# Performance work log

Hardware: AMD Instinct MI355X
Metric: run time of the kernel (lower is better)

## Reference

```python
import jax, jax.numpy as jnp
import numpy as np

NUM_HEADS = 16
EMBED = 1024
HEAD = EMBED // NUM_HEADS  # 64
MAX_DIST = 4
NEG_INF = -1e30


def setup_inputs() -> dict:
    key = jax.random.key(0)
    ks = jax.random.split(key, 8)
    B, S = 2, 2048
    x = jax.random.normal(ks[0], (B, S, EMBED), dtype=jnp.float32)
    return {
        "k": x,  # self-attention: k == v == q values
        "v": x,
        "q": x,
        "Wk": jax.random.normal(ks[1], (EMBED, EMBED), dtype=jnp.float32) * 0.02,
        "Wv": jax.random.normal(ks[2], (EMBED, EMBED), dtype=jnp.float32) * 0.02,
        "Wq": jax.random.normal(ks[3], (EMBED, EMBED), dtype=jnp.float32) * 0.02,
        "Wo": jax.random.normal(ks[4], (EMBED, EMBED), dtype=jnp.float32) * 0.02,
        "p_params": jax.random.normal(ks[5], (HEAD, 2 * MAX_DIST + 1), dtype=jnp.float32) * 0.02,
    }


def reference(k, v, q, Wk, Wv, Wq, Wo, p_params):
    B, Kl, _ = k.shape
    Ql = q.shape[1]
    # torch nn.Linear(bias=False): y = x @ W.T
    kh = (k @ Wk.T).reshape(B, Kl, NUM_HEADS, HEAD).transpose(0, 2, 1, 3)
    vh = (v @ Wv.T).reshape(B, Kl, NUM_HEADS, HEAD).transpose(0, 2, 1, 3)
    qh = (q @ Wq.T).reshape(B, Ql, NUM_HEADS, HEAD).transpose(0, 2, 1, 3)
    qh = qh / jnp.sqrt(jnp.float32(HEAD))
    # content scores: [B,H,Q,K]
    scores0 = jnp.einsum("bhqd,bhkd->bhqk", qh, kh)
    # relative-position bias: q . p_params[:, r] for each bucket r, then gather per (i,j)
    bias = jnp.einsum("bhqd,dr->bhqr", qh, p_params)  # [B,H,Q,2M+1]
    d = jnp.clip(jnp.arange(Ql)[:, None] - jnp.arange(Kl)[None, :], -MAX_DIST, MAX_DIST) + MAX_DIST  # [Q,K]
    rel = bias[:, :, jnp.arange(Ql)[:, None], d]  # [B,H,Q,K]
    scores = scores0 + rel
    # causal mask
    causal = jnp.arange(Ql)[:, None] >= jnp.arange(Kl)[None, :]
    scores = jnp.where(causal[None, None], scores, NEG_INF)
    attn = jax.nn.softmax(scores, axis=-1)
    out = jnp.einsum("bhqk,bhkd->bhqd", attn, vh)
    out = out.transpose(0, 2, 1, 3).reshape(B, Ql, EMBED)
    return out @ Wo.T
```

## Files before the change

kernel.cpp:

```cpp
#include <hip/hip_runtime.h>


using short8  = __attribute__((ext_vector_type(8))) short;
using floatx4 = __attribute__((ext_vector_type(4))) float;
using float4v = __attribute__((ext_vector_type(4))) float;
using ushort4v = __attribute__((ext_vector_type(4))) unsigned short;
using uint2v  = __attribute__((ext_vector_type(2))) unsigned int;

#define LOG2E 1.4426950408889634f

__device__ __forceinline__ unsigned short f2bf(float f) {
  unsigned u = __float_as_uint(f);
  return (unsigned short)((u + 0x7FFFu + ((u >> 16) & 1u)) >> 16);
}
__device__ __forceinline__ float bf2f(unsigned short s) {
  return __uint_as_float(((unsigned)s) << 16);
}
__device__ __forceinline__ unsigned cvt_pk_bf16(float lo, float hi) {
  unsigned r;
  asm("v_cvt_pk_bf16_f32 %0, %1, %2" : "=v"(r) : "v"(lo), "v"(hi));
  return r;
}
__device__ __forceinline__ void gload_lds16(const void* g, void* l) {
  __builtin_amdgcn_global_load_lds(
      (const __attribute__((address_space(1))) unsigned int*)g,
      (__attribute__((address_space(3))) unsigned int*)l, 16, 0, 0);
}

__global__ void f2bf_all(const float* __restrict__ x, unsigned short* xo,
                         const float* __restrict__ w0, unsigned short* o0,
                         const float* __restrict__ w1, unsigned short* o1,
                         const float* __restrict__ w2, unsigned short* o2,
                         const float* __restrict__ w3, unsigned short* o3) {
  int i = blockIdx.x * 256 + threadIdx.x;
  const float* in;
  unsigned short* out;
  int off;
  if (i < (1 << 20)) {
    in = x; out = xo; off = i;
  } else {
    int j = i - (1 << 20);
    int s = j >> 18;
    off = j & ((1 << 18) - 1);
    switch (s) {
      case 0: in = w0; out = o0; break;
      case 1: in = w1; out = o1; break;
      case 2: in = w2; out = o2; break;
      default: in = w3; out = o3; break;
    }
  }
  float4v v = ((const float4v*)in)[off];
  ushort4v o;
  o[0] = f2bf(v[0]); o[1] = f2bf(v[1]); o[2] = f2bf(v[2]); o[3] = f2bf(v[3]);
  ((ushort4v*)out)[off] = o;
}

template <int TM>
__device__ __forceinline__ void gemm_core64(
    const unsigned short* __restrict__ A, const unsigned short* __restrict__ B,
    void* __restrict__ Cv, int N, int K, int mBase, int nBase, float alpha,
    bool outbf, unsigned short* As, unsigned short* Bs) {
  const int tid = threadIdx.x;
  const int lane = tid & 63;
  const int w = tid >> 6;
  const int wr = w >> 1, wc = w & 1;
  const int lr = lane & 15, lg = lane >> 4;
  constexpr int NMF = TM / 32;

  floatx4 acc[NMF][4] = {};

  for (int k0 = 0; k0 < K; k0 += 64) {
#pragma unroll
    for (int i = 0; i < TM / 32; ++i) {
      int idx = i * 256 + tid;
      int row = idx >> 3, pc = idx & 7;
      int cl = pc ^ (row & 7);
      gload_lds16(A + (size_t)(mBase + row) * K + k0 + cl * 8, As + idx * 8);
    }
#pragma unroll
    for (int i = 0; i < 4; ++i) {
      int idx = i * 256 + tid;
      int row = idx >> 3, pc = idx & 7;
      int cl = pc ^ (row & 7);
      gload_lds16(B + (size_t)(nBase + row) * K + k0 + cl * 8, Bs + idx * 8);
    }
    __syncthreads();
#pragma unroll
    for (int c = 0; c < 2; ++c) {
      short8 af[NMF], bfr[4];
#pragma unroll
      for (int mf = 0; mf < NMF; ++mf) {
        int row = wr * (TM / 2) + mf * 16 + lr;
        af[mf] = *(const short8*)(As + row * 64 + (((c * 4 + lg) ^ (lr & 7)) * 8));
      }
#pragma unroll
      for (int nf = 0; nf < 4; ++nf) {
        int row = wc * 64 + nf * 16 + lr;
        bfr[nf] = *(const short8*)(Bs + row * 64 + (((c * 4 + lg) ^ (lr & 7)) * 8));
      }
#pragma unroll
      for (int mf = 0; mf < NMF; ++mf)
#pragma unroll
        for (int nf = 0; nf < 4; ++nf)
          acc[mf][nf] = __builtin_amdgcn_mfma_f32_16x16x32_bf16(
              af[mf], bfr[nf], acc[mf][nf], 0, 0, 0);
    }
    __syncthreads();
  }

#pragma unroll
  for (int mf = 0; mf < NMF; ++mf)
#pragma unroll
    for (int nf = 0; nf < 4; ++nf)
#pragma unroll
      for (int r = 0; r < 4; ++r) {
        size_t row = (size_t)mBase + wr * (TM / 2) + mf * 16 + lg * 4 + r;
        size_t col = (size_t)nBase + wc * 64 + nf * 16 + lr;
        float v = acc[mf][nf][r] * alpha;
        if (outbf)
          ((unsigned short*)Cv)[row * (size_t)N + col] = f2bf(v);
        else
          ((float*)Cv)[row * (size_t)N + col] = v;
      }
}

__global__ __launch_bounds__(256, 2) void proj3_kern(
    const unsigned short* __restrict__ xbf, const unsigned short* __restrict__ wkb,
    unsigned short* __restrict__ khb,
    const unsigned short* __restrict__ wqb, unsigned short* __restrict__ qhb,
    const unsigned short* __restrict__ wvb, unsigned short* __restrict__ vtb) {
  __shared__ alignas(16) unsigned short As[128 * 64];
  __shared__ alignas(16) unsigned short Bs[128 * 64];
  int z = blockIdx.z;
  if (z == 0)
    gemm_core64<128>(xbf, wkb, khb, 1024, 1024, blockIdx.y * 128,
                     blockIdx.x * 128, 1.0f, true, As, Bs);
  else if (z == 1)
    gemm_core64<128>(xbf, wqb, qhb, 1024, 1024, blockIdx.y * 128,
                     blockIdx.x * 128, 0.125f, true, As, Bs);
  else
    gemm_core64<128>(wvb, xbf, vtb, 4096, 1024, blockIdx.x * 128,
                     blockIdx.y * 128, 1.0f, true, As, Bs);
}

__global__ __launch_bounds__(256, 2) void gemm_out_kern(
    const unsigned short* __restrict__ A, const unsigned short* __restrict__ B,
    float* __restrict__ C) {
  __shared__ alignas(16) unsigned short As[64 * 64];
  __shared__ alignas(16) unsigned short Bs[128 * 64];
  gemm_core64<64>(A, B, C, 1024, 1024, blockIdx.y * 64, blockIdx.x * 128,
                  1.0f, false, As, Bs);
}

#define ENC(qi, k0, k1, pp) ((qi) | ((k0) << 4) | ((k1) << 9) | ((pp) << 15))
__device__ const unsigned int UTAB[38] = {
    ENC(5, 0, 12, 63),  ENC(4, 0, 10, 63),  ENC(6, 0, 8, 0),
    ENC(7, 0, 8, 2),    ENC(7, 8, 16, 3),   ENC(8, 0, 8, 4),
    ENC(8, 8, 16, 5),   ENC(9, 0, 8, 7),    ENC(9, 8, 16, 8),
    ENC(10, 0, 8, 10),  ENC(10, 8, 16, 11), ENC(11, 0, 8, 13),
    ENC(11, 8, 16, 14), ENC(11, 16, 24, 15),ENC(12, 0, 8, 16),
    ENC(12, 8, 16, 17), ENC(12, 16, 24, 18),ENC(13, 0, 8, 20),
    ENC(13, 8, 16, 21), ENC(13, 16, 24, 22),ENC(14, 0, 8, 24),
    ENC(14, 8, 16, 25), ENC(14, 16, 24, 26),ENC(15, 0, 8, 28),
    ENC(15, 8, 16, 29), ENC(15, 16, 24, 30),ENC(15, 24, 32, 31),
    ENC(3, 0, 8, 63),   ENC(2, 0, 6, 63),   ENC(6, 8, 14, 1),
    ENC(10, 16, 22, 12),ENC(14, 24, 30, 27),ENC(1, 0, 4, 63),
    ENC(9, 16, 20, 9),  ENC(13, 24, 28, 23),ENC(0, 0, 2, 63),
    ENC(8, 16, 18, 6),  ENC(12, 24, 26, 19)};

__global__ __launch_bounds__(512, 4) void attn_kern(
    const unsigned short* __restrict__ qh,
    const unsigned short* __restrict__ kh,
    const unsigned short* __restrict__ vt,
    const float* __restrict__ pp,
    unsigned short* __restrict__ ao,
    unsigned short* __restrict__ opart,
    float* __restrict__ mbuf,
    float* __restrict__ lbuf) {
  __shared__ alignas(16) char smem[49152];
  unsigned short* QA  = (unsigned short*)smem;
  unsigned short* Ks1 = (unsigned short*)smem;
  unsigned short* Vs1 = (unsigned short*)(smem + 8192);
  unsigned short* Ks0 = (unsigned short*)(smem + 16384);
  unsigned short* Vs0 = (unsigned short*)(smem + 24576);
  unsigned short* Ps  = (unsigned short*)(smem + 32768);
  float* ppS   = (float*)(smem + 32768);
  float* biasT = (float*)(smem + 35072);

  const int tid = threadIdx.x;
  const int lane = tid & 63;
  const int w = tid >> 6;
  const int lr = lane & 15, lg = lane >> 4;
  const int hb = blockIdx.x;
  const int h = hb & 15, b = hb >> 4;

  const unsigned e = UTAB[blockIdx.y];
  const int qi = e & 15;
  const int k0t = (e >> 4) & 31;
  const int k1t = (e >> 9) & 63;
  const int pofs = (e >> 15) & 63;
  const bool partial = (pofs != 63);
  const int qbase = qi << 7;
  const size_t bsQ = (size_t)b * 2048 + qbase;

  const unsigned short* khB = kh + ((size_t)b * 2048) * 1024 + h * 64;
  const unsigned short* vtB = vt + ((size_t)h * 64) * 4096 + b * 2048;

  auto stage_kv = [&](int kbase, unsigned short* Kd, unsigned short* Vd) {
    int row = tid >> 3, pc = tid & 7;
    int cl = pc ^ (row & 7);
    gload_lds16(khB + ((size_t)(kbase + row) << 10) + cl * 8, Kd + tid * 8);
    gload_lds16(vtB + ((size_t)row << 12) + kbase + cl * 8, Vd + tid * 8);
  };

#pragma unroll
  for (int t = 0; t < 2; ++t) {
    int idx = t * 512 + tid;
    int row = idx >> 3, c8 = (idx & 7) * 8;
    gload_lds16(qh + (bsQ + row) * 1024 + h * 64 + c8, QA + idx * 8);
  }
  for (int idx = tid; idx < 576; idx += 512) {
    int r = idx >> 6, d = idx & 63;
    ppS[r * 64 + d] = pp[d * 9 + r];
  }
  stage_kv(k0t * 64, Ks0, Vs0);
  __syncthreads();

  const int qrowL = w * 16 + lr;
  short8 aq[2];
#pragma unroll
  for (int c = 0; c < 2; ++c)
    aq[c] = *(const short8*)(QA + qrowL * 64 + c * 32 + lg * 8);

  for (int idx = tid; idx < 640; idx += 512) {
    int row = idx / 5, rr = idx - row * 5;
    const unsigned short* qrow = QA + row * 64;
    const float* pr = ppS + (rr + 4) * 64;
    float s = 0.f;
#pragma unroll
    for (int d8 = 0; d8 < 8; ++d8) {
      short8 qv = *(const short8*)(qrow + d8 * 8);
#pragma unroll
      for (int j = 0; j < 8; ++j)
        s += bf2f((unsigned short)qv[j]) * pr[d8 * 8 + j];
    }
    biasT[row * 6 + rr] = s;
  }
  __syncthreads();

  const float b4 = biasT[qrowL * 6 + 0];
  const float b5 = biasT[qrowL * 6 + 1];
  const float b6 = biasT[qrowL * 6 + 2];
  const float b7 = biasT[qrowL * 6 + 3];
  const float b8 = biasT[qrowL * 6 + 4];
  __syncthreads();

  const int q_glob = qbase + w * 16 + lr;
  const int wqtop = qbase + w * 16 + 15;
  unsigned short* Pw = Ps + w * 1024;

  float m_run = -1e30f, l_run = 0.f;
  floatx4 o[4] = {};

  for (int kt = k0t; kt < k1t; ++kt) {
    const int kbase = kt * 64;
    const int cur = (kt - k0t) & 1;
    unsigned short* Kc = cur ? Ks1 : Ks0;
    unsigned short* Vc = cur ? Vs1 : Vs0;
    if (kt + 1 < k1t)
      stage_kv(kbase + 64, cur ? Ks0 : Ks1, cur ? Vs0 : Vs1);

    if (kbase <= wqtop) {
      floatx4 sa[4] = {};
      __builtin_amdgcn_s_setprio(1);
#pragma unroll
      for (int kf = 0; kf < 4; ++kf)
#pragma unroll
        for (int c = 0; c < 2; ++c) {
          int row = kf * 16 + lr;
          short8 ak = *(const short8*)(Kc + row * 64 +
                                       (((c * 4 + lg) ^ (lr & 7)) * 8));
          sa[kf] = __builtin_amdgcn_mfma_f32_16x16x32_bf16(ak, aq[c], sa[kf],
                                                           0, 0, 0);
        }
      __builtin_amdgcn_s_setprio(0);

      float bext;
      if (qbase + w * 16 >= kbase + 67) {
        bext = b8;
      } else {
        bext = 0.f;
#pragma unroll
        for (int kf = 0; kf < 4; ++kf)
#pragma unroll
          for (int r = 0; r < 4; ++r) {
            int dq = q_glob - (kbase + kf * 16 + lg * 4 + r);
            float bb = (dq >= 4) ? b8
                     : (dq == 0 ? b4 : (dq == 1 ? b5 : (dq == 2 ? b6 : b7)));
            sa[kf][r] = (dq < 0) ? -1e30f : (sa[kf][r] + bb);
          }
      }

      float mx = -1e30f;
#pragma unroll
      for (int kf = 0; kf < 4; ++kf)
#pragma unroll
        for (int r = 0; r < 4; ++r) mx = fmaxf(mx, sa[kf][r]);
      mx += bext;
      mx = fmaxf(mx, __shfl_xor(mx, 16, 64));
      mx = fmaxf(mx, __shfl_xor(mx, 32, 64));
      if (__any(mx > m_run + 8.f)) {
        float mn = fmaxf(m_run, mx);
        float al = __builtin_amdgcn_exp2f((m_run - mn) * LOG2E);
        m_run = mn;
        l_run *= al;
        float alo[4];
#pragma unroll
        for (int r = 0; r < 4; ++r) alo[r] = __shfl(al, lg * 4 + r, 64);
#pragma unroll
        for (int df = 0; df < 4; ++df)
#pragma unroll
          for (int r = 0; r < 4; ++r) o[df][r] *= alo[r];
      }

      const float c1 = (bext - m_run) * LOG2E;
      float rs = 0.f;
#pragma unroll
      for (int kf = 0; kf < 4; ++kf) {
        float p0 = __builtin_amdgcn_exp2f(fmaf(sa[kf][0], LOG2E, c1));
        float p1 = __builtin_amdgcn_exp2f(fmaf(sa[kf][1], LOG2E, c1));
        float p2 = __builtin_amdgcn_exp2f(fmaf(sa[kf][2], LOG2E, c1));
        float p3 = __builtin_amdgcn_exp2f(fmaf(sa[kf][3], LOG2E, c1));
        rs += (p0 + p1) + (p2 + p3);
        uint2v pk;
        pk[0] = cvt_pk_bf16(p0, p1);
        pk[1] = cvt_pk_bf16(p2, p3);
        int phys = (kf * 2 + (lg >> 1)) ^ (lr & 7);
        *(uint2v*)(Pw + lr * 64 + phys * 8 + (lg & 1) * 4) = pk;
      }
      rs += __shfl_xor(rs, 16, 64);
      rs += __shfl_xor(rs, 32, 64);
      l_run += rs;

      __builtin_amdgcn_s_setprio(1);
#pragma unroll
      for (int c = 0; c < 2; ++c) {
        short8 pa = *(const short8*)(Pw + lr * 64 +
                                     (((c * 4 + lg) ^ (lr & 7)) * 8));
#pragma unroll
        for (int df = 0; df < 4; ++df) {
          int row = df * 16 + lr;
          short8 bv = *(const short8*)(Vc + row * 64 +
                                       (((c * 4 + lg) ^ (lr & 7)) * 8));
          o[df] = __builtin_amdgcn_mfma_f32_16x16x32_bf16(pa, bv, o[df],
                                                          0, 0, 0);
        }
      }
      __builtin_amdgcn_s_setprio(0);
    }
    __syncthreads();
  }

  if (!partial) {
    float rl[4];
#pragma unroll
    for (int r = 0; r < 4; ++r)
      rl[r] = __builtin_amdgcn_rcpf(__shfl(l_run, lg * 4 + r, 64));
    const size_t outRow0 = bsQ + w * 16 + lg * 4;
#pragma unroll
    for (int df = 0; df < 4; ++df)
#pragma unroll
      for (int r = 0; r < 4; ++r)
        ao[(outRow0 + r) * 1024 + h * 64 + df * 16 + lr] =
            f2bf(o[df][r] * rl[r]);
  } else {
    const int pid = hb * 32 + pofs;
    unsigned short* op = opart + (size_t)pid * 8192;
#pragma unroll
    for (int df = 0; df < 4; ++df)
#pragma unroll
      for (int r = 0; r < 4; ++r)
        op[(w * 16 + lg * 4 + r) * 64 + df * 16 + lr] = f2bf(o[df][r]);
    if (lg == 0) {
      mbuf[pid * 128 + w * 16 + lr] = m_run;
      lbuf[pid * 128 + w * 16 + lr] = l_run;
    }
  }
}

__global__ void combine_kern(const unsigned short* __restrict__ opart,
                             const float* __restrict__ mbuf,
                             const float* __restrict__ lbuf,
                             unsigned short* __restrict__ ao) {
  const unsigned char NC[10] = {2, 2, 3, 3, 3, 3, 4, 4, 4, 4};
  const unsigned char PB[10] = {0, 2, 4, 7, 10, 13, 16, 20, 24, 28};
  const int bx = blockIdx.x;
  const int hb = bx / 10, ii = bx - hb * 10;
  const int i = 6 + ii;
  const int b = hb >> 4, h = hb & 15;
  const int nc = NC[ii];
  const int pid0 = hb * 32 + PB[ii];
  const int row = threadIdx.x >> 1;
  const int colg = (threadIdx.x & 1) * 32;

  float m[4], l[4];
  float M = -1e30f;
  for (int c = 0; c < nc; ++c) {
    m[c] = mbuf[(pid0 + c) * 128 + row];
    l[c] = lbuf[(pid0 + c) * 128 + row];
    M = fmaxf(M, m[c]);
  }
  float s[4], lsum = 0.f;
  for (int c = 0; c < nc; ++c) {
    s[c] = __builtin_amdgcn_exp2f((m[c] - M) * LOG2E);
    lsum = fmaf(l[c], s[c], lsum);
  }
  const float linv = 1.f / lsum;

  unsigned short* dst =
      ao + ((size_t)b * 2048 + i * 128 + row) * 1024 + h * 64 + colg;
#pragma unroll
  for (int t = 0; t < 4; ++t) {
    float acc[8] = {};
    for (int c = 0; c < nc; ++c) {
      const unsigned short* Oc =
          opart + (size_t)(pid0 + c) * 8192 + row * 64 + colg + t * 8;
      short8 a = *(const short8*)Oc;
#pragma unroll
      for (int j = 0; j < 8; ++j)
        acc[j] = fmaf(bf2f((unsigned short)a[j]), s[c], acc[j]);
    }
    short8 ov;
#pragma unroll
    for (int j = 0; j < 8; ++j) ov[j] = (short)f2bf(acc[j] * linv);
    *(short8*)(dst + t * 8) = ov;
  }
}

extern "C" void kernel_launch(void* const* d_in, const int* in_sizes, int n_in,
                              void* d_out, int out_size, void* d_ws,
                              size_t ws_size, hipStream_t stream) {
  const float* k_in = (const float*)d_in[0];
  const float* Wk = (const float*)d_in[3];
  const float* Wv = (const float*)d_in[4];
  const float* Wq = (const float*)d_in[5];
  const float* Wo = (const float*)d_in[6];
  const float* pp = (const float*)d_in[7];

  const size_t NX = 4096u * 1024u;
  const size_t NW = 1024u * 1024u;
  unsigned short* ws = (unsigned short*)d_ws;
  unsigned short* xbf = ws;
  unsigned short* wkb = xbf + NX;
  unsigned short* wvb = wkb + NW;
  unsigned short* wqb = wvb + NW;
  unsigned short* wob = wqb + NW;
  unsigned short* khb = wob + NW;
  unsigned short* vtb = khb + NX;
  unsigned short* qhb = vtb + NX;
  unsigned short* aob = qhb + NX;
  unsigned short* opart = aob + NX;
  float* mbuf = (float*)xbf;
  float* lbuf = mbuf + 1024 * 128;

  (void)in_sizes; (void)n_in; (void)out_size; (void)ws_size;

  f2bf_all<<<dim3(8192), dim3(256), 0, stream>>>(
      k_in, xbf, Wk, wkb, Wv, wvb, Wq, wqb, Wo, wob);

  proj3_kern<<<dim3(8, 32, 3), dim3(256), 0, stream>>>(
      xbf, wkb, khb, wqb, qhb, wvb, vtb);

  attn_kern<<<dim3(32, 38), dim3(512), 0, stream>>>(qhb, khb, vtb, pp, aob,
                                                    opart, mbuf, lbuf);
  combine_kern<<<dim3(320), dim3(256), 0, stream>>>(opart, mbuf, lbuf, aob);

  gemm_out_kern<<<dim3(8, 64), dim3(256), 0, stream>>>(aob, wob, (float*)d_out);
}
```

Baseline: 112.5 us.

## Halve attention block threads, each wave handles two query tiles with register-staged KV

The attention kernel now runs 256 threads per block, and each wave processes 32 query rows as two 16-row sub-tiles. This lets every K and V fragment loaded from LDS feed two MFMAs instead of one, cutting LDS read traffic per unit of work. K/V staging changes from direct global-to-LDS loads to a register prefetch two tiles ahead, written to LDS one tile ahead, and the loop-end sync becomes an explicit lgkmcnt wait plus barrier. In exchange the kernel uses more registers per thread and has fewer waves per block, which can reduce latency hiding.

```diff
diff --git a/kernel.cpp b/kernel.cpp
--- a/kernel.cpp
+++ b/kernel.cpp
@@ -168,7 +168,7 @@
     ENC(9, 16, 20, 9),  ENC(13, 24, 28, 23),ENC(0, 0, 2, 63),
     ENC(8, 16, 18, 6),  ENC(12, 24, 26, 19)};
 
-__global__ __launch_bounds__(512, 4) void attn_kern(
+__global__ __launch_bounds__(256, 3) void attn_kern(
     const unsigned short* __restrict__ qh,
     const unsigned short* __restrict__ kh,
     const unsigned short* __restrict__ vt,
@@ -206,33 +206,56 @@
   const unsigned short* khB = kh + ((size_t)b * 2048) * 1024 + h * 64;
   const unsigned short* vtB = vt + ((size_t)h * 64) * 4096 + b * 2048;
 
-  auto stage_kv = [&](int kbase, unsigned short* Kd, unsigned short* Vd) {
-    int row = tid >> 3, pc = tid & 7;
-    int cl = pc ^ (row & 7);
-    gload_lds16(khB + ((size_t)(kbase + row) << 10) + cl * 8, Kd + tid * 8);
-    gload_lds16(vtB + ((size_t)row << 12) + kbase + cl * 8, Vd + tid * 8);
+  const int srow0 = tid >> 3, spc = tid & 7;
+  const int scl0 = spc ^ (srow0 & 7);
+  const int srow1 = srow0 + 32;
+  const int scl1 = spc ^ (srow1 & 7);
+
+  auto stage_kv_lds = [&](int kbase, unsigned short* Kd, unsigned short* Vd) {
+    gload_lds16(khB + ((size_t)(kbase + srow0) << 10) + scl0 * 8, Kd + tid * 8);
+    gload_lds16(vtB + ((size_t)srow0 << 12) + kbase + scl0 * 8, Vd + tid * 8);
+    gload_lds16(khB + ((size_t)(kbase + srow1) << 10) + scl1 * 8,
+                Kd + (256 + tid) * 8);
+    gload_lds16(vtB + ((size_t)srow1 << 12) + kbase + scl1 * 8,
+                Vd + (256 + tid) * 8);
   };
 
-#pragma unroll
-  for (int t = 0; t < 2; ++t) {
-    int idx = t * 512 + tid;
+  short8 kreg0, kreg1, vreg0, vreg1;
+  auto load_regs = [&](int kbase) {
+    kreg0 = *(const short8*)(khB + ((size_t)(kbase + srow0) << 10) + scl0 * 8);
+    vreg0 = *(const short8*)(vtB + ((size_t)srow0 << 12) + kbase + scl0 * 8);
+    kreg1 = *(const short8*)(khB + ((size_t)(kbase + srow1) << 10) + scl1 * 8);
+    vreg1 = *(const short8*)(vtB + ((size_t)srow1 << 12) + kbase + scl1 * 8);
+  };
+  auto write_regs = [&](unsigned short* Kd, unsigned short* Vd) {
+    *(short8*)(Kd + tid * 8) = kreg0;
+    *(short8*)(Vd + tid * 8) = vreg0;
+    *(short8*)(Kd + (256 + tid) * 8) = kreg1;
+    *(short8*)(Vd + (256 + tid) * 8) = vreg1;
+  };
+
+#pragma unroll
+  for (int t = 0; t < 4; ++t) {
+    int idx = t * 256 + tid;
     int row = idx >> 3, c8 = (idx & 7) * 8;
     gload_lds16(qh + (bsQ + row) * 1024 + h * 64 + c8, QA + idx * 8);
   }
-  for (int idx = tid; idx < 576; idx += 512) {
+  for (int idx = tid; idx < 576; idx += 256) {
     int r = idx >> 6, d = idx & 63;
     ppS[r * 64 + d] = pp[d * 9 + r];
   }
-  stage_kv(k0t * 64, Ks0, Vs0);
+  stage_kv_lds(k0t * 64, Ks0, Vs0);
   __syncthreads();
 
-  const int qrowL = w * 16 + lr;
-  short8 aq[2];
-#pragma unroll
-  for (int c = 0; c < 2; ++c)
-    aq[c] = *(const short8*)(QA + qrowL * 64 + c * 32 + lg * 8);
-
-  for (int idx = tid; idx < 640; idx += 512) {
+  const int qr0 = w * 32 + lr, qr1 = qr0 + 16;
+  short8 aq0[2], aq1[2];
+#pragma unroll
+  for (int c = 0; c < 2; ++c) {
+    aq0[c] = *(const short8*)(QA + qr0 * 64 + c * 32 + lg * 8);
+    aq1[c] = *(const short8*)(QA + qr1 * 64 + c * 32 + lg * 8);
+  }
+
+  for (int idx = tid; idx < 640; idx += 256) {
     int row = idx / 5, rr = idx - row * 5;
     const unsigned short* qrow = QA + row * 64;
     const float* pr = ppS + (rr + 4) * 64;
@@ -248,30 +271,35 @@
   }
   __syncthreads();
 
-  const float b4 = biasT[qrowL * 6 + 0];
-  const float b5 = biasT[qrowL * 6 + 1];
-  const float b6 = biasT[qrowL * 6 + 2];
-  const float b7 = biasT[qrowL * 6 + 3];
-  const float b8 = biasT[qrowL * 6 + 4];
+  float bia0[5], bia1[5];
+#pragma unroll
+  for (int r = 0; r < 5; ++r) {
+    bia0[r] = biasT[qr0 * 6 + r];
+    bia1[r] = biasT[qr1 * 6 + r];
+  }
   __syncthreads();
 
-  const int q_glob = qbase + w * 16 + lr;
-  const int wqtop = qbase + w * 16 + 15;
-  unsigned short* Pw = Ps + w * 1024;
-
-  float m_run = -1e30f, l_run = 0.f;
-  floatx4 o[4] = {};
+  const int qg0 = qbase + qr0, qg1 = qbase + qr1;
+  unsigned short* Pw = Ps + w * 2048;
+
+  if (k0t + 1 < k1t) load_regs((k0t + 1) * 64);
+
+  float m0 = -1e30f, l0 = 0.f, m1 = -1e30f, l1 = 0.f;
+  floatx4 o0[4] = {}, o1[4] = {};
 
   for (int kt = k0t; kt < k1t; ++kt) {
     const int kbase = kt * 64;
     const int cur = (kt - k0t) & 1;
     unsigned short* Kc = cur ? Ks1 : Ks0;
     unsigned short* Vc = cur ? Vs1 : Vs0;
-    if (kt + 1 < k1t)
-      stage_kv(kbase + 64, cur ? Ks0 : Ks1, cur ? Vs0 : Vs1);
-
-    if (kbase <= wqtop) {
-      floatx4 sa[4] = {};
+
+    if (kt + 1 < k1t) write_regs(cur ? Ks0 : Ks1, cur ? Vs0 : Vs1);
+    if (kt + 2 < k1t) load_regs(kbase + 128);
+
+    if (kbase <= qbase + w * 32 + 31) {
+      const bool live0 = (kbase <= qbase + w * 32 + 15);
+
+      floatx4 sa0[4] = {}, sa1[4] = {};
       __builtin_amdgcn_s_setprio(1);
 #pragma unroll
       for (int kf = 0; kf < 4; ++kf)
@@ -280,110 +308,189 @@
           int row = kf * 16 + lr;
           short8 ak = *(const short8*)(Kc + row * 64 +
                                        (((c * 4 + lg) ^ (lr & 7)) * 8));
-          sa[kf] = __builtin_amdgcn_mfma_f32_16x16x32_bf16(ak, aq[c], sa[kf],
-                                                           0, 0, 0);
+          if (live0)
+            sa0[kf] = __builtin_amdgcn_mfma_f32_16x16x32_bf16(ak, aq0[c],
+                                                              sa0[kf], 0, 0, 0);
+          sa1[kf] = __builtin_amdgcn_mfma_f32_16x16x32_bf16(ak, aq1[c],
+                                                            sa1[kf], 0, 0, 0);
         }
       __builtin_amdgcn_s_setprio(0);
 
-      float bext;
-      if (qbase + w * 16 >= kbase + 67) {
-        bext = b8;
+      float bex1;
+      if (qbase + w * 32 + 16 >= kbase + 67) {
+        bex1 = bia1[4];
       } else {
-        bext = 0.f;
+        bex1 = 0.f;
 #pragma unroll
         for (int kf = 0; kf < 4; ++kf)
 #pragma unroll
           for (int r = 0; r < 4; ++r) {
-            int dq = q_glob - (kbase + kf * 16 + lg * 4 + r);
-            float bb = (dq >= 4) ? b8
-                     : (dq == 0 ? b4 : (dq == 1 ? b5 : (dq == 2 ? b6 : b7)));
-            sa[kf][r] = (dq < 0) ? -1e30f : (sa[kf][r] + bb);
+            int dq = qg1 - (kbase + kf * 16 + lg * 4 + r);
+            float bb = (dq >= 4) ? bia1[4]
+                     : (dq == 0 ? bia1[0] : (dq == 1 ? bia1[1]
+                     : (dq == 2 ? bia1[2] : bia1[3])));
+            sa1[kf][r] = (dq < 0) ? -1e30f : (sa1[kf][r] + bb);
           }
       }
-
-      float mx = -1e30f;
+      float mx1 = -1e30f;
 #pragma unroll
       for (int kf = 0; kf < 4; ++kf)
 #pragma unroll
-        for (int r = 0; r < 4; ++r) mx = fmaxf(mx, sa[kf][r]);
-      mx += bext;
-      mx = fmaxf(mx, __shfl_xor(mx, 16, 64));
-      mx = fmaxf(mx, __shfl_xor(mx, 32, 64));
-      if (__any(mx > m_run + 8.f)) {
-        float mn = fmaxf(m_run, mx);
-        float al = __builtin_amdgcn_exp2f((m_run - mn) * LOG2E);
-        m_run = mn;
-        l_run *= al;
+        for (int r = 0; r < 4; ++r) mx1 = fmaxf(mx1, sa1[kf][r]);
+      mx1 += bex1;
+      mx1 = fmaxf(mx1, __shfl_xor(mx1, 16, 64));
+      mx1 = fmaxf(mx1, __shfl_xor(mx1, 32, 64));
+      if (__any(mx1 > m1 + 8.f)) {
+        float mn = fmaxf(m1, mx1);
+        float al = __builtin_amdgcn_exp2f((m1 - mn) * LOG2E);
+        m1 = mn;
+        l1 *= al;
         float alo[4];
 #pragma unroll
         for (int r = 0; r < 4; ++r) alo[r] = __shfl(al, lg * 4 + r, 64);
 #pragma unroll
         for (int df = 0; df < 4; ++df)
 #pragma unroll
-          for (int r = 0; r < 4; ++r) o[df][r] *= alo[r];
-      }
-
-      const float c1 = (bext - m_run) * LOG2E;
-      float rs = 0.f;
-#pragma unroll
-      for (int kf = 0; kf < 4; ++kf) {
-        float p0 = __builtin_amdgcn_exp2f(fmaf(sa[kf][0], LOG2E, c1));
-        float p1 = __builtin_amdgcn_exp2f(fmaf(sa[kf][1], LOG2E, c1));
-        float p2 = __builtin_amdgcn_exp2f(fmaf(sa[kf][2], LOG2E, c1));
-        float p3 = __builtin_amdgcn_exp2f(fmaf(sa[kf][3], LOG2E, c1));
-        rs += (p0 + p1) + (p2 + p3);
-        uint2v pk;
-        pk[0] = cvt_pk_bf16(p0, p1);
-        pk[1] = cvt_pk_bf16(p2, p3);
-        int phys = (kf * 2 + (lg >> 1)) ^ (lr & 7);
-        *(uint2v*)(Pw + lr * 64 + phys * 8 + (lg & 1) * 4) = pk;
-      }
-      rs += __shfl_xor(rs, 16, 64);
-      rs += __shfl_xor(rs, 32, 64);
-      l_run += rs;
-
+          for (int r = 0; r < 4; ++r) o1[df][r] *= alo[r];
+      }
+      {
+        const float c1 = (bex1 - m1) * LOG2E;
+        float rs = 0.f;
+#pragma unroll
+        for (int kf = 0; kf < 4; ++kf) {
+          float p0 = __builtin_amdgcn_exp2f(fmaf(sa1[kf][0], LOG2E, c1));
+          float p1 = __builtin_amdgcn_exp2f(fmaf(sa1[kf][1], LOG2E, c1));
+          float p2 = __builtin_amdgcn_exp2f(fmaf(sa1[kf][2], LOG2E, c1));
+          float p3 = __builtin_amdgcn_exp2f(fmaf(sa1[kf][3], LOG2E, c1));
+          rs += (p0 + p1) + (p2 + p3);
+          uint2v pk;
+          pk[0] = cvt_pk_bf16(p0, p1);
+          pk[1] = cvt_pk_bf16(p2, p3);
+          int phys = (kf * 2 + (lg >> 1)) ^ (lr & 7);
+          *(uint2v*)(Pw + 1024 + lr * 64 + phys * 8 + (lg & 1) * 4) = pk;
+        }
+        rs += __shfl_xor(rs, 16, 64);
+        rs += __shfl_xor(rs, 32, 64);
+        l1 += rs;
+      }
+
+      if (live0) {
+        float bex0;
+        if (qbase + w * 32 >= kbase + 67) {
+          bex0 = bia0[4];
+        } else {
+          bex0 = 0.f;
+#pragma unroll
+          for (int kf = 0; kf < 4; ++kf)
+#pragma unroll
+            for (int r = 0; r < 4; ++r) {
+              int dq = qg0 - (kbase + kf * 16 + lg * 4 + r);
+              float bb = (dq >= 4) ? bia0[4]
+                       : (dq == 0 ? bia0[0] : (dq == 1 ? bia0[1]
+                       : (dq == 2 ? bia0[2] : bia0[3])));
+              sa0[kf][r] = (dq < 0) ? -1e30f : (sa0[kf][r] + bb);
+            }
+        }
+        float mx0 = -1e30f;
+#pragma unroll
+        for (int kf = 0; kf < 4; ++kf)
+#pragma unroll
+          for (int r = 0; r < 4; ++r) mx0 = fmaxf(mx0, sa0[kf][r]);
+        mx0 += bex0;
+        mx0 = fmaxf(mx0, __shfl_xor(mx0, 16, 64));
+        mx0 = fmaxf(mx0, __shfl_xor(mx0, 32, 64));
+        if (__any(mx0 > m0 + 8.f)) {
+          float mn = fmaxf(m0, mx0);
+          float al = __builtin_amdgcn_exp2f((m0 - mn) * LOG2E);
+          m0 = mn;
+          l0 *= al;
+          float alo[4];
+#pragma unroll
+          for (int r = 0; r < 4; ++r) alo[r] = __shfl(al, lg * 4 + r, 64);
+#pragma unroll
+          for (int df = 0; df < 4; ++df)
+#pragma unroll
+            for (int r = 0; r < 4; ++r) o0[df][r] *= alo[r];
+        }
+        const float c1 = (bex0 - m0) * LOG2E;
+        float rs = 0.f;
+#pragma unroll
+        for (int kf = 0; kf < 4; ++kf) {
+          float p0 = __builtin_amdgcn_exp2f(fmaf(sa0[kf][0], LOG2E, c1));
+          float p1 = __builtin_amdgcn_exp2f(fmaf(sa0[kf][1], LOG2E, c1));
+          float p2 = __builtin_amdgcn_exp2f(fmaf(sa0[kf][2], LOG2E, c1));
+          float p3 = __builtin_amdgcn_exp2f(fmaf(sa0[kf][3], LOG2E, c1));
+          rs += (p0 + p1) + (p2 + p3);
+          uint2v pk;
+          pk[0] = cvt_pk_bf16(p0, p1);
+          pk[1] = cvt_pk_bf16(p2, p3);
+          int phys = (kf * 2 + (lg >> 1)) ^ (lr & 7);
+          *(uint2v*)(Pw + lr * 64 + phys * 8 + (lg & 1) * 4) = pk;
+        }
+        rs += __shfl_xor(rs, 16, 64);
+        rs += __shfl_xor(rs, 32, 64);
+        l0 += rs;
+      }
+
+      short8 pa0[2], pa1[2];
+#pragma unroll
+      for (int c = 0; c < 2; ++c) {
+        int off = lr * 64 + (((c * 4 + lg) ^ (lr & 7)) * 8);
+        if (live0) pa0[c] = *(const short8*)(Pw + off);
+        pa1[c] = *(const short8*)(Pw + 1024 + off);
+      }
       __builtin_amdgcn_s_setprio(1);
 #pragma unroll
-      for (int c = 0; c < 2; ++c) {
-        short8 pa = *(const short8*)(Pw + lr * 64 +
-                                     (((c * 4 + lg) ^ (lr & 7)) * 8));
+      for (int c = 0; c < 2; ++c)
 #pragma unroll
         for (int df = 0; df < 4; ++df) {
           int row = df * 16 + lr;
           short8 bv = *(const short8*)(Vc + row * 64 +
                                        (((c * 4 + lg) ^ (lr & 7)) * 8));
-          o[df] = __builtin_amdgcn_mfma_f32_16x16x32_bf16(pa, bv, o[df],
-                                                          0, 0, 0);
+          if (live0)
+            o0[df] = __builtin_amdgcn_mfma_f32_16x16x32_bf16(pa0[c], bv,
+                                                             o0[df], 0, 0, 0);
+          o1[df] = __builtin_amdgcn_mfma_f32_16x16x32_bf16(pa1[c], bv,
+                                                           o1[df], 0, 0, 0);
         }
-      }
       __builtin_amdgcn_s_setprio(0);
     }
-    __syncthreads();
+
+    asm volatile("s_waitcnt lgkmcnt(0)" ::: "memory");
+    __builtin_amdgcn_s_barrier();
   }
 
   if (!partial) {
-    float rl[4];
-#pragma unroll
-    for (int r = 0; r < 4; ++r)
-      rl[r] = __builtin_amdgcn_rcpf(__shfl(l_run, lg * 4 + r, 64));
-    const size_t outRow0 = bsQ + w * 16 + lg * 4;
+    float rl0[4], rl1[4];
+#pragma unroll
+    for (int r = 0; r < 4; ++r) {
+      rl0[r] = __builtin_amdgcn_rcpf(__shfl(l0, lg * 4 + r, 64));
+      rl1[r] = __builtin_amdgcn_rcpf(__shfl(l1, lg * 4 + r, 64));
+    }
+    const size_t row0 = bsQ + w * 32 + lg * 4;
 #pragma unroll
     for (int df = 0; df < 4; ++df)
 #pragma unroll
-      for (int r = 0; r < 4; ++r)
-        ao[(outRow0 + r) * 1024 + h * 64 + df * 16 + lr] =
-            f2bf(o[df][r] * rl[r]);
+      for (int r = 0; r < 4; ++r) {
+        ao[(row0 + r) * 1024 + h * 64 + df * 16 + lr] = f2bf(o0[df][r] * rl0[r]);
+        ao[(row0 + 16 + r) * 1024 + h * 64 + df * 16 + lr] =
+            f2bf(o1[df][r] * rl1[r]);
+      }
   } else {
     const int pid = hb * 32 + pofs;
     unsigned short* op = opart + (size_t)pid * 8192;
 #pragma unroll
     for (int df = 0; df < 4; ++df)
 #pragma unroll
-      for (int r = 0; r < 4; ++r)
-        op[(w * 16 + lg * 4 + r) * 64 + df * 16 + lr] = f2bf(o[df][r]);
+      for (int r = 0; r < 4; ++r) {
+        op[(w * 32 + lg * 4 + r) * 64 + df * 16 + lr] = f2bf(o0[df][r]);
+        op[(w * 32 + 16 + lg * 4 + r) * 64 + df * 16 + lr] = f2bf(o1[df][r]);
+      }
     if (lg == 0) {
-      mbuf[pid * 128 + w * 16 + lr] = m_run;
-      lbuf[pid * 128 + w * 16 + lr] = l_run;
+      mbuf[pid * 128 + w * 32 + lr] = m0;
+      lbuf[pid * 128 + w * 32 + lr] = l0;
+      mbuf[pid * 128 + w * 32 + 16 + lr] = m1;
+      lbuf[pid * 128 + w * 32 + 16 + lr] = l1;
     }
   }
 }
@@ -471,7 +578,7 @@
   proj3_kern<<<dim3(8, 32, 3), dim3(256), 0, stream>>>(
       xbf, wkb, khb, wqb, qhb, wvb, vtb);
 
-  attn_kern<<<dim3(32, 38), dim3(512), 0, stream>>>(qhb, khb, vtb, pp, aob,
+  attn_kern<<<dim3(32, 38), dim3(256), 0, stream>>>(qhb, khb, vtb, pp, aob,
                                                     opart, mbuf, lbuf);
   combine_kern<<<dim3(320), dim3(256), 0, stream>>>(opart, mbuf, lbuf, aob);
 
```

After: 124.8 us. 11.0% more time.
